# Optimization experiments

Measured on AMD Instinct MI355X. Metric: run time of the kernel, lower is better.

The kernel has to match this reference:

```python
import jax, jax.numpy as jnp
import numpy as np

EMBED_DIM = 1024
NUM_HEADS = 16
HEAD_DIM = EMBED_DIM // NUM_HEADS


def setup_inputs() -> dict:
    key = jax.random.key(0)
    ks = jax.random.split(key, 7)
    B, S, D = 2, 2048, EMBED_DIM
    s = 1.0 / np.sqrt(D)
    return {
        "x": jax.random.normal(ks[0], (B, S, D), dtype=jnp.float32),
        "Wq": jax.random.normal(ks[1], (D, D), dtype=jnp.float32) * s,
        "bq": jax.random.normal(ks[2], (D,), dtype=jnp.float32) * 0.01,
        "Wk": jax.random.normal(ks[3], (D, D), dtype=jnp.float32) * s,
        "bk": jax.random.normal(ks[4], (D,), dtype=jnp.float32) * 0.01,
        "Wv": jax.random.normal(ks[5], (D, D), dtype=jnp.float32) * s,
        "bv": jax.random.normal(ks[6], (D,), dtype=jnp.float32) * 0.01,
    }


def reference(x, Wq, bq, Wk, bk, Wv, bv):
    B, S, D = x.shape
    H, Hd = NUM_HEADS, HEAD_DIM
    # QKV projections, then split heads: [B, S, D] -> [B, H, S, Hd]
    q = (x @ Wq + bq).reshape(B, S, H, Hd).transpose(0, 2, 1, 3)
    k = (x @ Wk + bk).reshape(B, S, H, Hd).transpose(0, 2, 1, 3)
    v = (x @ Wv + bv).reshape(B, S, H, Hd).transpose(0, 2, 1, 3)
    # NOTE: the original module applies NO 1/sqrt(head_dim) scaling.
    energy = jnp.einsum("bhqd,bhkd->bhqk", q, k)  # [B, H, S, S]
    attn = jax.nn.softmax(energy, axis=-1)
    out = jnp.einsum("bhqk,bhkd->bhqd", attn, v)
    return out.transpose(0, 2, 1, 3).reshape(B, S, D)
```

## Files before the change

### kernel.cpp

```cpp
#include <hip/hip_runtime.h>
#include <stdint.h>
#include <stddef.h>

typedef _Float16 half_t;
typedef __attribute__((ext_vector_type(8))) _Float16 h16x8;
typedef __attribute__((ext_vector_type(4))) _Float16 h16x4;
typedef __attribute__((ext_vector_type(4))) float f32x4;

#define MFMA16(a, b, c) __builtin_amdgcn_mfma_f32_16x16x32_f16(a, b, c, 0, 0, 0)
#define EXP2(x) __builtin_amdgcn_exp2f(x)

#define SW(row, slot) ((((slot) ^ ((row) & 7))) * 8)

__global__ __launch_bounds__(256) void cvt_x_kernel(const float* __restrict__ x,
                                                    half_t* __restrict__ xh, int n8) {
    int i = blockIdx.x * blockDim.x + threadIdx.x;
    if (i >= n8) return;
    const float4* xv = (const float4*)x;
    float4 a = xv[i * 2 + 0];
    float4 b = xv[i * 2 + 1];
    h16x8 o;
    o[0] = (half_t)a.x; o[1] = (half_t)a.y; o[2] = (half_t)a.z; o[3] = (half_t)a.w;
    o[4] = (half_t)b.x; o[5] = (half_t)b.y; o[6] = (half_t)b.z; o[7] = (half_t)b.w;
    ((h16x8*)xh)[i] = o;
}

__global__ __launch_bounds__(256) void cvt_w_kernel(const float* __restrict__ Wq,
                                                    const float* __restrict__ Wk,
                                                    const float* __restrict__ Wv,
                                                    half_t* __restrict__ Wt) {
    __shared__ float t[32][33];
    const float* W = (blockIdx.z == 0) ? Wq : ((blockIdx.z == 1) ? Wk : Wv);
    int k0 = blockIdx.y * 32, n0 = blockIdx.x * 32;
    int tid = threadIdx.x;
    int r = tid >> 3;
    int c4 = (tid & 7) * 4;
    float4 v = *(const float4*)&W[(size_t)(k0 + r) * 1024 + n0 + c4];
    t[r][c4 + 0] = v.x; t[r][c4 + 1] = v.y; t[r][c4 + 2] = v.z; t[r][c4 + 3] = v.w;
    __syncthreads();
    half_t* o = Wt + (size_t)blockIdx.z * 1024 * 1024 + (size_t)(n0 + r) * 1024 + k0 + c4;
    h16x4 h;
    h[0] = (half_t)t[c4 + 0][r];
    h[1] = (half_t)t[c4 + 1][r];
    h[2] = (half_t)t[c4 + 2][r];
    h[3] = (half_t)t[c4 + 3][r];
    *(h16x4*)o = h;
}

__global__ __launch_bounds__(256, 2) void gemm_qkv_kernel(
    const half_t* __restrict__ xh,
    const half_t* __restrict__ Wt,
    const float* __restrict__ bq, const float* __restrict__ bk,
    const float* __restrict__ bv,
    half_t* __restrict__ qkv)
{
    const int p = blockIdx.z;
    const float* bias = (p == 0) ? bq : ((p == 1) ? bk : bv);
    const half_t* Wp = Wt + (size_t)p * 1024 * 1024;
    const int n0 = blockIdx.x * 128, m0 = blockIdx.y * 128;

    __shared__ half_t Al[128][72];
    __shared__ half_t Bl[128][72];

    const int tid = threadIdx.x;
    const int lane = tid & 63, wid = tid >> 6;
    const int wm = wid >> 1, wn = wid & 1;
    const int g = lane >> 4, r = lane & 15;

    const int srow = tid >> 3;
    const int scol = (tid & 7) * 8;

    f32x4 acc[4][4];
#pragma unroll
    for (int a = 0; a < 4; a++)
#pragma unroll
        for (int c = 0; c < 4; c++) acc[a][c] = (f32x4){0.f, 0.f, 0.f, 0.f};

    h16x8 ra[4], rb[4];
#pragma unroll
    for (int i = 0; i < 4; i++) {
        ra[i] = *(const h16x8*)&xh[(size_t)(m0 + srow + i * 32) * 1024 + scol];
        rb[i] = *(const h16x8*)&Wp[(size_t)(n0 + srow + i * 32) * 1024 + scol];
    }

    for (int k0 = 0; k0 < 1024; k0 += 64) {
        __syncthreads();
#pragma unroll
        for (int i = 0; i < 4; i++) {
            *(h16x8*)&Al[srow + i * 32][scol] = ra[i];
            *(h16x8*)&Bl[srow + i * 32][scol] = rb[i];
        }
        __syncthreads();

        int kn = (k0 + 64) & 1023;
#pragma unroll
        for (int i = 0; i < 4; i++) {
            ra[i] = *(const h16x8*)&xh[(size_t)(m0 + srow + i * 32) * 1024 + kn + scol];
            rb[i] = *(const h16x8*)&Wp[(size_t)(n0 + srow + i * 32) * 1024 + kn + scol];
        }

#pragma unroll
        for (int t = 0; t < 2; t++) {
            h16x8 af[4], bf[4];
#pragma unroll
            for (int mi = 0; mi < 4; mi++)
                af[mi] = *(const h16x8*)&Al[wm * 64 + mi * 16 + r][t * 32 + g * 8];
#pragma unroll
            for (int ni = 0; ni < 4; ni++)
                bf[ni] = *(const h16x8*)&Bl[wn * 64 + ni * 16 + r][t * 32 + g * 8];
#pragma unroll
            for (int mi = 0; mi < 4; mi++)
#pragma unroll
                for (int ni = 0; ni < 4; ni++)
                    acc[mi][ni] = MFMA16(af[mi], bf[ni], acc[mi][ni]);
        }
    }

    float bn[4];
#pragma unroll
    for (int ni = 0; ni < 4; ni++) bn[ni] = bias[n0 + wn * 64 + ni * 16 + r];

    if (p == 0) {
        half_t* outp = qkv;
#pragma unroll
        for (int mi = 0; mi < 4; mi++) {
#pragma unroll
            for (int ni = 0; ni < 4; ni++) {
                int n = n0 + wn * 64 + ni * 16 + r;
                int hq = n >> 6, hd = n & 63;
#pragma unroll
                for (int i = 0; i < 4; i++) {
                    int m = m0 + wm * 64 + mi * 16 + g * 4 + i;
                    int b = m >> 11, s = m & 2047;
                    outp[(((size_t)(b * 16 + hq) * 2048 + s) << 6) + hd] =
                        (half_t)(acc[mi][ni][i] + bn[ni]);
                }
            }
        }
    } else if (p == 1) {
        half_t* outp = qkv + (size_t)4194304;
        const int kt = ((m0 & 2047) + wm * 64) >> 6;
        const int bK = (m0 + wm * 64) >> 11;
#pragma unroll
        for (int ni = 0; ni < 4; ni++) {
            int n = n0 + wn * 64 + ni * 16 + r;
            int hK = n >> 6, hd = n & 63;
            int tt = hd >> 5, ggk = (hd >> 3) & 3, jK = hd & 7;
            size_t base = (size_t)(bK * 16 + hK) * 131072 + kt * 4096 + tt * 512 + ggk * 128 + jK;
#pragma unroll
            for (int mi = 0; mi < 4; mi++)
#pragma unroll
                for (int i = 0; i < 4; i++)
                    outp[base + mi * 1024 + (g * 4 + i) * 8] =
                        (half_t)(acc[mi][ni][i] + bn[ni]);
        }
    } else {
        half_t* outp = qkv + (size_t)2 * 4194304;
        const int kt = ((m0 & 2047) + wm * 64) >> 6;
        const int bV = (m0 + wm * 64) >> 11;
        const int jv = (g & 1) * 4, gv_hi = g >> 1;
#pragma unroll
        for (int ni = 0; ni < 4; ni++) {
            int n = n0 + wn * 64 + ni * 16 + r;
            int hV = n >> 6;
            size_t hb = (size_t)(bV * 16 + hV) * 131072 + kt * 4096 + ni * 1024;
#pragma unroll
            for (int mi = 0; mi < 4; mi++) {
                int ks = mi >> 1, ggv = (mi & 1) * 2 + gv_hi;
                h16x4 pk;
#pragma unroll
                for (int i = 0; i < 4; i++) pk[i] = (half_t)(acc[mi][ni][i] + bn[ni]);
                *(h16x4*)&outp[hb + ks * 512 + ggv * 128 + r * 8 + jv] = pk;
            }
        }
    }
}

__global__ __launch_bounds__(256, 2) void attn_kernel(
    const half_t* __restrict__ Qg,
    const half_t* __restrict__ Kswz,
    const half_t* __restrict__ Vswz,
    float* __restrict__ out)
{
    __shared__ half_t Pl[4][32][64];

    const int tid = threadIdx.x;
    const int lane = tid & 63, wid = tid >> 6;
    const int g = lane >> 4, r = lane & 15;

    const int bid = blockIdx.x;
    const int xcd = bid & 7;
    const int t_  = bid >> 3;
    const int qblk = t_ & 15;
    const int bh = xcd + 8 * (t_ >> 4);

    const int b = bh >> 4, h = bh & 15;
    const half_t* Qb = Qg + (size_t)bh * 131072;
    const half_t* Kp = Kswz + (size_t)bh * 131072;
    const half_t* Vp = Vswz + (size_t)bh * 131072;
    const int q0 = qblk * 128 + wid * 32;
    const int lofs = g * 128 + r * 8;

    h16x8 qf[2][2];
#pragma unroll
    for (int qg = 0; qg < 2; qg++)
#pragma unroll
        for (int t = 0; t < 2; t++) {
            qf[qg][t] = *(const h16x8*)&Qb[(size_t)(q0 + qg * 16 + r) * 64 + t * 32 + g * 8];
            qf[qg][t] *= (half_t)1.44269504f;
        }

    f32x4 o[2][4];
#pragma unroll
    for (int qg = 0; qg < 2; qg++)
#pragma unroll
        for (int d = 0; d < 4; d++) o[qg][d] = (f32x4){0.f, 0.f, 0.f, 0.f};
    float m_run[2] = {0.f, 0.f}, l_run[2] = {0.f, 0.f};

    h16x8 kf[8], vf[8];

    auto loadK = [&](int kt) {
#pragma unroll
        for (int kc = 0; kc < 4; kc++)
#pragma unroll
            for (int t = 0; t < 2; t++)
                kf[kc * 2 + t] = *(const h16x8*)&Kp[kt * 4096 + kc * 1024 + t * 512 + lofs];
    };
    auto loadV = [&](int kt) {
#pragma unroll
        for (int d = 0; d < 4; d++)
#pragma unroll
            for (int ks = 0; ks < 2; ks++)
                vf[d * 2 + ks] = *(const h16x8*)&Vp[kt * 4096 + d * 1024 + ks * 512 + lofs];
    };

    auto QKT = [&](f32x4 (&e)[2][4]) {
#pragma unroll
        for (int kc = 0; kc < 4; kc++) {
            e[0][kc] = (f32x4){0.f, 0.f, 0.f, 0.f};
            e[1][kc] = (f32x4){0.f, 0.f, 0.f, 0.f};
#pragma unroll
            for (int t = 0; t < 2; t++) {
                e[0][kc] = MFMA16(kf[kc * 2 + t], qf[0][t], e[0][kc]);
                e[1][kc] = MFMA16(kf[kc * 2 + t], qf[1][t], e[1][kc]);
            }
        }
    };

    auto SOFTMAX_P = [&](f32x4 (&e)[2][4]) {
#pragma unroll
        for (int qg = 0; qg < 2; qg++) {
            float t0 = fmaxf(fmaxf(e[qg][0][0], e[qg][0][1]), e[qg][0][2]);
            float t1 = fmaxf(fmaxf(e[qg][0][3], e[qg][1][0]), e[qg][1][1]);
            float t2 = fmaxf(fmaxf(e[qg][1][2], e[qg][1][3]), e[qg][2][0]);
            float t3 = fmaxf(fmaxf(e[qg][2][1], e[qg][2][2]), e[qg][2][3]);
            float t4 = fmaxf(fmaxf(e[qg][3][0], e[qg][3][1]), e[qg][3][2]);
            float tm = fmaxf(fmaxf(t0, t1), fmaxf(fmaxf(t2, t3), fmaxf(t4, e[qg][3][3])));
            tm = fmaxf(tm, __shfl_xor(tm, 16));
            tm = fmaxf(tm, __shfl_xor(tm, 32));

            float ps0 = 0.f, ps1 = 0.f, ps2 = 0.f, ps3 = 0.f;
#pragma unroll
            for (int i = 0; i < 4; i++) { e[qg][0][i] = EXP2(e[qg][0][i] - m_run[qg]); ps0 += e[qg][0][i]; }
#pragma unroll
            for (int i = 0; i < 4; i++) { e[qg][1][i] = EXP2(e[qg][1][i] - m_run[qg]); ps1 += e[qg][1][i]; }
#pragma unroll
            for (int i = 0; i < 4; i++) { e[qg][2][i] = EXP2(e[qg][2][i] - m_run[qg]); ps2 += e[qg][2][i]; }
#pragma unroll
            for (int i = 0; i < 4; i++) { e[qg][3][i] = EXP2(e[qg][3][i] - m_run[qg]); ps3 += e[qg][3][i]; }

            if (!__all(tm <= m_run[qg] + 8.f)) {
                float nm = fmaxf(m_run[qg], tm);
                float sc = EXP2(m_run[qg] - nm);
                m_run[qg] = nm;
                l_run[qg] *= sc;
#pragma unroll
                for (int kc = 0; kc < 4; kc++)
#pragma unroll
                    for (int i = 0; i < 4; i++) e[qg][kc][i] *= sc;
                ps0 *= sc; ps1 *= sc; ps2 *= sc; ps3 *= sc;
#pragma unroll
                for (int i = 0; i < 4; i++) {
                    float sci = __shfl(sc, (lane & 48) | (g * 4 + i));
#pragma unroll
                    for (int d = 0; d < 4; d++) o[qg][d][i] *= sci;
                }
            }

            l_run[qg] += (ps0 + ps1) + (ps2 + ps3);

#pragma unroll
            for (int kc = 0; kc < 4; kc++) {
                h16x4 pk;
#pragma unroll
                for (int i = 0; i < 4; i++) pk[i] = (half_t)e[qg][kc][i];
                *(h16x4*)&Pl[wid][qg * 16 + r][SW(r, 2 * kc + (g >> 1)) + (g & 1) * 4] = pk;
            }
        }
    };

    auto PV = [&]() {
        asm volatile("s_waitcnt lgkmcnt(0)" ::: "memory");
        __builtin_amdgcn_sched_barrier(0);
#pragma unroll
        for (int ks = 0; ks < 2; ks++) {
            h16x8 pf0 = *(const h16x8*)&Pl[wid][r][SW(r, ks * 4 + g)];
            h16x8 pf1 = *(const h16x8*)&Pl[wid][16 + r][SW(r, ks * 4 + g)];
#pragma unroll
            for (int d = 0; d < 4; d++) {
                o[0][d] = MFMA16(pf0, vf[d * 2 + ks], o[0][d]);
                o[1][d] = MFMA16(pf1, vf[d * 2 + ks], o[1][d]);
            }
        }
    };

    f32x4 eA[2][4], eB[2][4];
    loadK(0);
    QKT(eA);
    loadK(1);

    for (int kt = 0; kt < 32; kt += 2) {
        loadV(kt);
        QKT(eB);
        loadK((kt + 2) & 31);
        SOFTMAX_P(eA);
        PV();
        loadV(kt + 1);
        QKT(eA);
        loadK((kt + 3) & 31);
        SOFTMAX_P(eB);
        PV();
    }

#pragma unroll
    for (int qg = 0; qg < 2; qg++) {
        float lr = l_run[qg];
        lr += __shfl_xor(lr, 16);
        lr += __shfl_xor(lr, 32);
#pragma unroll
        for (int i = 0; i < 4; i++) {
            float li = __shfl(lr, (lane & 48) | (g * 4 + i));
            float inv = 1.0f / li;
            int s = q0 + qg * 16 + g * 4 + i;
            float* op = out + (size_t)(b * 2048 + s) * 1024 + h * 64 + r;
#pragma unroll
            for (int d = 0; d < 4; d++) op[d * 16] = o[qg][d][i] * inv;
        }
    }
}

extern "C" void kernel_launch(void* const* d_in, const int* in_sizes, int n_in,
                              void* d_out, int out_size, void* d_ws, size_t ws_size,
                              hipStream_t stream) {
    const float* x  = (const float*)d_in[0];
    const float* Wq = (const float*)d_in[1];
    const float* bq = (const float*)d_in[2];
    const float* Wk = (const float*)d_in[3];
    const float* bk = (const float*)d_in[4];
    const float* Wv = (const float*)d_in[5];
    const float* bv = (const float*)d_in[6];
    float* out = (float*)d_out;

    half_t* xh  = (half_t*)d_ws;
    half_t* Wt  = (half_t*)((char*)d_ws + (size_t)8 * 1024 * 1024);
    half_t* qkv = (half_t*)((char*)d_ws + (size_t)14 * 1024 * 1024);
    half_t* Qh  = qkv;
    half_t* Kh  = qkv + (size_t)4194304;
    half_t* Vth = qkv + (size_t)8388608;

    cvt_x_kernel<<<2048, 256, 0, stream>>>(x, xh, 524288);
    cvt_w_kernel<<<dim3(32, 32, 3), 256, 0, stream>>>(Wq, Wk, Wv, Wt);
    gemm_qkv_kernel<<<dim3(8, 32, 3), 256, 0, stream>>>(xh, Wt, bq, bk, bv, qkv);
    attn_kernel<<<512, 256, 0, stream>>>(Qh, Kh, Vth, out);
}
```

Baseline: 105.2 us.

## Use direct global-to-LDS loads in QKV GEMM and compute softmax row sums via MFMA

The QKV projection GEMM now loads its tiles with global_load_lds straight into swizzled, unpadded shared memory and no longer prefetches through registers. Occupancy is raised to 3 blocks per CU. In the attention kernel, the per-lane softmax row-sum adds and final shuffles are replaced by an extra MFMA of P against a vector of ones, so the sums come out already in the output layout. The GEMM loses its register prefetch overlap between tiles, and the attention kernel gains two MFMAs per PV step in exchange for fewer VALU adds.

```diff
diff --git a/kernel.cpp b/kernel.cpp
--- a/kernel.cpp
+++ b/kernel.cpp
@@ -11,6 +11,12 @@
 #define EXP2(x) __builtin_amdgcn_exp2f(x)
 
 #define SW(row, slot) ((((slot) ^ ((row) & 7))) * 8)
+
+__device__ __forceinline__ void gload_lds16(const half_t* g, half_t* l) {
+    __builtin_amdgcn_global_load_lds(
+        (const __attribute__((address_space(1))) void*)g,
+        (__attribute__((address_space(3))) void*)l, 16, 0, 0);
+}
 
 __global__ __launch_bounds__(256) void cvt_x_kernel(const float* __restrict__ x,
                                                     half_t* __restrict__ xh, int n8) {
@@ -47,7 +53,7 @@
     *(h16x4*)o = h;
 }
 
-__global__ __launch_bounds__(256, 2) void gemm_qkv_kernel(
+__global__ __launch_bounds__(256, 3) void gemm_qkv_kernel(
     const half_t* __restrict__ xh,
     const half_t* __restrict__ Wt,
     const float* __restrict__ bq, const float* __restrict__ bk,
@@ -59,55 +65,43 @@
     const half_t* Wp = Wt + (size_t)p * 1024 * 1024;
     const int n0 = blockIdx.x * 128, m0 = blockIdx.y * 128;
 
-    __shared__ half_t Al[128][72];
-    __shared__ half_t Bl[128][72];
+    __shared__ half_t Al[128][64];
+    __shared__ half_t Bl[128][64];
 
     const int tid = threadIdx.x;
     const int lane = tid & 63, wid = tid >> 6;
     const int wm = wid >> 1, wn = wid & 1;
     const int g = lane >> 4, r = lane & 15;
 
-    const int srow = tid >> 3;
-    const int scol = (tid & 7) * 8;
+    const int lrow = lane >> 3;
+    const int swzc = ((lane & 7) ^ lrow) * 8;
 
     f32x4 acc[4][4];
 #pragma unroll
     for (int a = 0; a < 4; a++)
 #pragma unroll
         for (int c = 0; c < 4; c++) acc[a][c] = (f32x4){0.f, 0.f, 0.f, 0.f};
-
-    h16x8 ra[4], rb[4];
-#pragma unroll
-    for (int i = 0; i < 4; i++) {
-        ra[i] = *(const h16x8*)&xh[(size_t)(m0 + srow + i * 32) * 1024 + scol];
-        rb[i] = *(const h16x8*)&Wp[(size_t)(n0 + srow + i * 32) * 1024 + scol];
-    }
 
     for (int k0 = 0; k0 < 1024; k0 += 64) {
         __syncthreads();
 #pragma unroll
-        for (int i = 0; i < 4; i++) {
-            *(h16x8*)&Al[srow + i * 32][scol] = ra[i];
-            *(h16x8*)&Bl[srow + i * 32][scol] = rb[i];
+        for (int j = 0; j < 4; j++) {
+            int issue = wid * 4 + j;
+            int row = issue * 8 + lrow;
+            gload_lds16(&xh[(size_t)(m0 + row) * 1024 + k0 + swzc], &Al[0][0] + issue * 512);
+            gload_lds16(&Wp[(size_t)(n0 + row) * 1024 + k0 + swzc], &Bl[0][0] + issue * 512);
         }
         __syncthreads();
-
-        int kn = (k0 + 64) & 1023;
-#pragma unroll
-        for (int i = 0; i < 4; i++) {
-            ra[i] = *(const h16x8*)&xh[(size_t)(m0 + srow + i * 32) * 1024 + kn + scol];
-            rb[i] = *(const h16x8*)&Wp[(size_t)(n0 + srow + i * 32) * 1024 + kn + scol];
-        }
 
 #pragma unroll
         for (int t = 0; t < 2; t++) {
             h16x8 af[4], bf[4];
 #pragma unroll
             for (int mi = 0; mi < 4; mi++)
-                af[mi] = *(const h16x8*)&Al[wm * 64 + mi * 16 + r][t * 32 + g * 8];
+                af[mi] = *(const h16x8*)&Al[wm * 64 + mi * 16 + r][SW(r, t * 4 + g)];
 #pragma unroll
             for (int ni = 0; ni < 4; ni++)
-                bf[ni] = *(const h16x8*)&Bl[wn * 64 + ni * 16 + r][t * 32 + g * 8];
+                bf[ni] = *(const h16x8*)&Bl[wn * 64 + ni * 16 + r][SW(r, t * 4 + g)];
 #pragma unroll
             for (int mi = 0; mi < 4; mi++)
 #pragma unroll
@@ -210,12 +204,17 @@
             qf[qg][t] *= (half_t)1.44269504f;
         }
 
-    f32x4 o[2][4];
-#pragma unroll
-    for (int qg = 0; qg < 2; qg++)
+    const h16x8 ones = {(half_t)1.f, (half_t)1.f, (half_t)1.f, (half_t)1.f,
+                        (half_t)1.f, (half_t)1.f, (half_t)1.f, (half_t)1.f};
+
+    f32x4 o[2][4], lsum[2];
+#pragma unroll
+    for (int qg = 0; qg < 2; qg++) {
 #pragma unroll
         for (int d = 0; d < 4; d++) o[qg][d] = (f32x4){0.f, 0.f, 0.f, 0.f};
-    float m_run[2] = {0.f, 0.f}, l_run[2] = {0.f, 0.f};
+        lsum[qg] = (f32x4){0.f, 0.f, 0.f, 0.f};
+    }
+    float m_run[2] = {0.f, 0.f};
 
     h16x8 kf[8], vf[8];
 
@@ -259,35 +258,27 @@
             tm = fmaxf(tm, __shfl_xor(tm, 16));
             tm = fmaxf(tm, __shfl_xor(tm, 32));
 
-            float ps0 = 0.f, ps1 = 0.f, ps2 = 0.f, ps3 = 0.f;
-#pragma unroll
-            for (int i = 0; i < 4; i++) { e[qg][0][i] = EXP2(e[qg][0][i] - m_run[qg]); ps0 += e[qg][0][i]; }
-#pragma unroll
-            for (int i = 0; i < 4; i++) { e[qg][1][i] = EXP2(e[qg][1][i] - m_run[qg]); ps1 += e[qg][1][i]; }
-#pragma unroll
-            for (int i = 0; i < 4; i++) { e[qg][2][i] = EXP2(e[qg][2][i] - m_run[qg]); ps2 += e[qg][2][i]; }
-#pragma unroll
-            for (int i = 0; i < 4; i++) { e[qg][3][i] = EXP2(e[qg][3][i] - m_run[qg]); ps3 += e[qg][3][i]; }
+#pragma unroll
+            for (int kc = 0; kc < 4; kc++)
+#pragma unroll
+                for (int i = 0; i < 4; i++) e[qg][kc][i] = EXP2(e[qg][kc][i] - m_run[qg]);
 
             if (!__all(tm <= m_run[qg] + 8.f)) {
                 float nm = fmaxf(m_run[qg], tm);
                 float sc = EXP2(m_run[qg] - nm);
                 m_run[qg] = nm;
-                l_run[qg] *= sc;
 #pragma unroll
                 for (int kc = 0; kc < 4; kc++)
 #pragma unroll
                     for (int i = 0; i < 4; i++) e[qg][kc][i] *= sc;
-                ps0 *= sc; ps1 *= sc; ps2 *= sc; ps3 *= sc;
 #pragma unroll
                 for (int i = 0; i < 4; i++) {
                     float sci = __shfl(sc, (lane & 48) | (g * 4 + i));
+                    lsum[qg][i] *= sci;
 #pragma unroll
                     for (int d = 0; d < 4; d++) o[qg][d][i] *= sci;
                 }
             }
-
-            l_run[qg] += (ps0 + ps1) + (ps2 + ps3);
 
 #pragma unroll
             for (int kc = 0; kc < 4; kc++) {
@@ -311,6 +302,8 @@
                 o[0][d] = MFMA16(pf0, vf[d * 2 + ks], o[0][d]);
                 o[1][d] = MFMA16(pf1, vf[d * 2 + ks], o[1][d]);
             }
+            lsum[0] = MFMA16(pf0, ones, lsum[0]);
+            lsum[1] = MFMA16(pf1, ones, lsum[1]);
         }
     };
 
@@ -333,20 +326,15 @@
     }
 
 #pragma unroll
-    for (int qg = 0; qg < 2; qg++) {
-        float lr = l_run[qg];
-        lr += __shfl_xor(lr, 16);
-        lr += __shfl_xor(lr, 32);
+    for (int qg = 0; qg < 2; qg++)
 #pragma unroll
         for (int i = 0; i < 4; i++) {
-            float li = __shfl(lr, (lane & 48) | (g * 4 + i));
-            float inv = 1.0f / li;
+            float inv = 1.0f / lsum[qg][i];
             int s = q0 + qg * 16 + g * 4 + i;
             float* op = out + (size_t)(b * 2048 + s) * 1024 + h * 64 + r;
 #pragma unroll
             for (int d = 0; d < 4; d++) op[d * 16] = o[qg][d][i] * inv;
         }
-    }
 }
 
 extern "C" void kernel_launch(void* const* d_in, const int* in_sizes, int n_in,
```

After: 101.6 us. 3.4% less time.
